# Performance work log

Measured on AMD Instinct MI355X. Metric: run time of the kernel, lower is better.

The kernel has to match this reference:

```python
import jax, jax.numpy as jnp
import numpy as np

B, S, D, H = 1, 2048, 1024, 16
DEPTH = D // H          # 64
A_DFF = 1024
NRES = 2                # num_reslayerA
SLOPE = 0.2             # LeakyReLU slope in plga attention
POW_EPS = 1e-9


def _ln(x, g, b):
    m = jnp.mean(x, axis=-1, keepdims=True)
    v = jnp.var(x, axis=-1, keepdims=True)
    return (x - m) * jax.lax.rsqrt(v + 1e-6) * g + b


def setup_inputs() -> dict:
    key = jax.random.key(0)
    ks = jax.random.split(key, 12)
    s = 0.02
    W = lambda k, shp: jax.random.normal(k, shp, jnp.float32) * s
    return {
        'q': jax.random.normal(ks[0], (B, S, D), jnp.float32),
        'k': jax.random.normal(ks[1], (B, S, D), jnp.float32),
        'v': jax.random.normal(ks[2], (B, S, D), jnp.float32),
        'mask': jnp.zeros((B, 1, 1, S), jnp.float32),
        'wq_w': W(ks[3], (D, D)), 'wq_b': jnp.zeros((D,), jnp.float32),
        'wk_w': W(ks[4], (D, D)), 'wk_b': jnp.zeros((D,), jnp.float32),
        'wv_w': W(ks[5], (D, D)), 'wv_b': jnp.zeros((D,), jnp.float32),
        'wo_w': W(ks[6], (D, D)), 'wo_b': jnp.zeros((D,), jnp.float32),
        # stacked ResLayerA params: Dense(depth->A_dff, relu) -> Dense(A_dff->depth) -> LN
        'rl_w1': W(ks[7], (NRES, DEPTH, A_DFF)), 'rl_b1': jnp.zeros((NRES, A_DFF), jnp.float32),
        'rl_w2': W(ks[8], (NRES, A_DFF, DEPTH)), 'rl_b2': jnp.zeros((NRES, DEPTH), jnp.float32),
        'rl_g': jnp.ones((NRES, DEPTH), jnp.float32), 'rl_beta': jnp.zeros((NRES, DEPTH), jnp.float32),
        # plga layer params: power coefficients, attention vector, bias
        'pw': jnp.ones((DEPTH,), jnp.float32),
        'a_vec': W(ks[9], (DEPTH,)),
        'ba': jnp.zeros((), jnp.float32),
    }


def reference(q, k, v, mask, wq_w, wq_b, wk_w, wk_b, wv_w, wv_b, wo_w, wo_b,
              rl_w1, rl_b1, rl_w2, rl_b2, rl_g, rl_beta, pw, a_vec, ba):
    Bq = q.shape[0]
    split = lambda x: x.reshape(Bq, -1, H, DEPTH).transpose(0, 2, 1, 3)  # [b,h,s,d]
    qh = split(q @ wq_w + wq_b)
    kh = split(k @ wk_w + wk_b)
    vh = split(v @ wv_w + wv_b)

    # metric tensor A = q^T q  -> [b,h,depth,depth]
    A = jnp.einsum('bhsd,bhse->bhde', qh, qh)
    # ResLayerA residual dense+LN stack over last dim
    for i in range(NRES):
        Ain = A
        hdn = jax.nn.relu(A @ rl_w1[i] + rl_b1[i])
        A = _ln((hdn @ rl_w2[i] + rl_b2[i]) + Ain, rl_g[i], rl_beta[i])

    # power-law graph attention (plga_layer, att_head=1, activation=None)
    Ap = jnp.power(jnp.abs(A) + POW_EPS, pw)                  # element-wise learned power
    avAp = jnp.einsum('d,bhde->bhe', a_vec, Ap)               # [b,h,depth] per-dim scaling
    E = jnp.einsum('bhsd,bhd,bhtd->bhst', qh, avAp, kh)       # pairwise logits [b,h,s,s]
    Ep = jnp.where(E > 0, E, SLOPE * E) + ba                  # LeakyReLU + learned bias
    Ep = Ep + mask * (-1e9)
    attv = jax.nn.softmax(Ep, axis=-1)
    Hnext = jnp.einsum('bhst,bhtd->bhsd', attv, vh)

    Hnext = Hnext.transpose(0, 2, 1, 3).reshape(Bq, -1, D)
    out = Hnext @ wo_w + wo_b
    return (out, E, A, pw, attv, ba, avAp, Ep)
```

## Files before the change

### kernel.cpp

```cpp
#include <hip/hip_runtime.h>
#include <stdint.h>

#define S_ 2048
#define D_ 1024
#define H_ 16
#define DEP_ 64

typedef float f32x4 __attribute__((ext_vector_type(4)));
typedef __bf16 bf16x8 __attribute__((ext_vector_type(8)));

#define MFMA16(a,b,c) __builtin_amdgcn_mfma_f32_16x16x32_bf16((a),(b),(c),0,0,0)

static constexpr size_t OFF_E    = 2097152ull;
static constexpr size_t OFF_A    = 69206016ull;
static constexpr size_t OFF_PW   = 69271552ull;
static constexpr size_t OFF_ATT  = 69271616ull;
static constexpr size_t OFF_BA   = 136380480ull;
static constexpr size_t OFF_AVAP = 136380481ull;
static constexpr size_t OFF_EP   = 136381505ull;

__device__ __forceinline__ short f2b(float f) {
  union { float f; uint32_t u; } c; c.f = f;
  uint32_t u = c.u;
  uint32_t r = (u + 0x7fffu + ((u >> 16) & 1u)) >> 16;
  return (short)(r & 0xffffu);
}
__device__ __forceinline__ float b2f(short s) {
  union { uint32_t u; float f; } c; c.u = ((uint32_t)(uint16_t)s) << 16;
  return c.f;
}
__device__ __forceinline__ void st_nt(float* p, f32x4 v) {
  __builtin_nontemporal_store(v, (f32x4*)p);
}

__global__ void k_cvt_all(const float* __restrict__ q, const float* __restrict__ k,
                          const float* __restrict__ v, const float* __restrict__ wq,
                          const float* __restrict__ wk, const float* __restrict__ wv,
                          const float* __restrict__ wo, const float* __restrict__ w1,
                          const float* __restrict__ w2, short* __restrict__ xbf,
                          short* __restrict__ wT, short* __restrict__ w1T,
                          short* __restrict__ w2T) {
  __shared__ float tile[64][65];
  int bid = blockIdx.x, t = threadIdx.x;
  if (bid < 6144) {
    int z = bid >> 11, bx = bid & 2047;
    const float* src = (z == 0) ? q : (z == 1) ? k : v;
    short* d = xbf + (size_t)z * (S_*D_);
    int i = (bx*256 + t)*4;
    float4 f = *(const float4*)(src + i);
    short4 o;
    o.x = f2b(f.x); o.y = f2b(f.y); o.z = f2b(f.z); o.w = f2b(f.w);
    *(short4*)(d + i) = o;
  } else if (bid < 7168) {
    int u = bid - 6144, z = u >> 8, tl = u & 255;
    int k0 = (tl >> 4)*64, n0 = (tl & 15)*64;
    const float* W = (z == 0) ? wq : (z == 1) ? wk : (z == 2) ? wv : wo;
    short* d = wT + (size_t)z * (D_*D_);
    for (int i = 0; i < 16; ++i) {
      int e = i*256 + t, r = e >> 6, c = e & 63;
      tile[r][c] = W[(size_t)(k0+r)*D_ + n0 + c];
    }
    __syncthreads();
    for (int i = 0; i < 16; ++i) {
      int e = i*256 + t, r = e >> 6, c = e & 63;
      d[(size_t)(n0+r)*D_ + k0 + c] = f2b(tile[c][r]);
    }
  } else {
    int u = bid - 7168, z = u >> 4, bx = u & 15;
    int l = z >> 1, which = z & 1;
    if (which == 0) {
      const float* src = w1 + (size_t)l*65536;
      short* d = w1T + (size_t)l*65536;
      int n0 = bx*64;
      for (int i = 0; i < 16; ++i) {
        int e = i*256 + t, r = e >> 6, c = e & 63;
        tile[r][c] = src[(size_t)r*1024 + n0 + c];
      }
      __syncthreads();
      for (int i = 0; i < 16; ++i) {
        int e = i*256 + t, r = e >> 6, c = e & 63;
        d[(size_t)(n0+r)*64 + c] = f2b(tile[c][r]);
      }
    } else {
      const float* src = w2 + (size_t)l*65536;
      short* d = w2T + (size_t)l*65536;
      int k0 = bx*64;
      for (int i = 0; i < 16; ++i) {
        int e = i*256 + t, r = e >> 6, c = e & 63;
        tile[r][c] = src[(size_t)(k0+r)*64 + c];
      }
      __syncthreads();
      for (int i = 0; i < 16; ++i) {
        int e = i*256 + t, r = e >> 6, c = e & 63;
        d[(size_t)r*1024 + k0 + c] = f2b(tile[c][r]);
      }
    }
  }
}

__global__ __launch_bounds__(256) void k_gemm(
    const short* __restrict__ Xall, const short* __restrict__ X2,
    const short* __restrict__ X3, const short* __restrict__ X4,
    const short* __restrict__ WTall,
    const float* __restrict__ b0, const float* __restrict__ b1v,
    const float* __restrict__ b2v, short* __restrict__ dstall,
    float* __restrict__ outf, int mode) {
  __shared__ __align__(16) short SS[2*128*72];
  short* As = SS;
  short* Bs = SS + 128*72;
  int z = blockIdx.z;
  const short* X  = Xall + (size_t)z * (S_*D_);
  const short* WT = WTall + (size_t)z * (D_*D_);
  int m0 = blockIdx.x * 128, n0 = blockIdx.y * 128;
  int t = threadIdx.x, lane = t & 63;
  int wr = t >> 7, wc = (t >> 6) & 1;
  int rA = lane & 15, kg = lane >> 4;
  f32x4 acc[4][4] = {};
  for (int kt = 0; kt < 16; ++kt) {
#pragma unroll
    for (int i = 0; i < 4; ++i) {
      int cid = i*256 + t, row = cid >> 3, c = cid & 7;
      size_t xi = (size_t)(m0+row)*D_ + kt*64 + c*8;
      if (mode == 2) {
        union { int4 v; short s[8]; } a1, a2, a3, a4, o;
        a1.v = *(const int4*)&X[xi];
        a2.v = *(const int4*)&X2[xi];
        a3.v = *(const int4*)&X3[xi];
        a4.v = *(const int4*)&X4[xi];
#pragma unroll
        for (int j = 0; j < 8; ++j)
          o.s[j] = f2b(b2f(a1.s[j]) + b2f(a2.s[j]) + b2f(a3.s[j]) + b2f(a4.s[j]));
        *(int4*)&As[row*72 + c*8] = o.v;
      } else {
        *(int4*)&As[row*72 + c*8] = *(const int4*)&X[xi];
      }
      *(int4*)&Bs[row*72 + c*8] = *(const int4*)&WT[(size_t)(n0+row)*D_ + kt*64 + c*8];
    }
    __syncthreads();
#pragma unroll
    for (int kk = 0; kk < 2; ++kk) {
      bf16x8 a[4], b[4];
#pragma unroll
      for (int m = 0; m < 4; ++m)
        a[m] = *(const bf16x8*)&As[(wr*64 + m*16 + rA)*72 + kk*32 + kg*8];
#pragma unroll
      for (int n = 0; n < 4; ++n)
        b[n] = *(const bf16x8*)&Bs[(wc*64 + n*16 + rA)*72 + kk*32 + kg*8];
#pragma unroll
      for (int m = 0; m < 4; ++m)
#pragma unroll
        for (int n = 0; n < 4; ++n)
          acc[m][n] = MFMA16(a[m], b[n], acc[m][n]);
    }
    __syncthreads();
  }
  const float* bias = (mode != 0) ? b0 : (z == 0 ? b0 : (z == 1 ? b1v : b2v));
  if (mode == 0) {
    short* Ct = SS;
#pragma unroll
    for (int m = 0; m < 4; ++m)
#pragma unroll
      for (int n = 0; n < 4; ++n) {
        int col = wc*64 + n*16 + rA;
        float bb = bias[n0 + col];
#pragma unroll
        for (int rr = 0; rr < 4; ++rr) {
          int row = wr*64 + m*16 + kg*4 + rr;
          Ct[row*136 + col] = f2b(acc[m][n][rr] + bb);
        }
      }
    __syncthreads();
#pragma unroll
    for (int p = 0; p < 8; ++p) {
      int row = p*16 + (t >> 4), unit = t & 15;
      int4 vv = *(const int4*)&Ct[row*136 + unit*8];
      int gcol = n0 + unit*8;
      int head = gcol >> 6, dd = gcol & 63;
      *(int4*)&dstall[(size_t)z*(S_*D_) + ((size_t)head*S_ + m0 + row)*DEP_ + dd] = vv;
    }
  } else {
    float* Ct = (float*)SS;
#pragma unroll
    for (int half = 0; half < 2; ++half) {
      if (wr == half) {
#pragma unroll
        for (int m = 0; m < 4; ++m)
#pragma unroll
          for (int n = 0; n < 4; ++n) {
            int col = wc*64 + n*16 + rA;
            float bb = bias[n0 + col];
#pragma unroll
            for (int rr = 0; rr < 4; ++rr)
              Ct[(m*16 + kg*4 + rr)*132 + col] = acc[m][n][rr] + bb;
          }
      }
      __syncthreads();
#pragma unroll
      for (int p = 0; p < 8; ++p) {
        int row_l = p*8 + (t >> 5), unit = t & 31;
        f32x4 vv = *(const f32x4*)&Ct[row_l*132 + unit*4];
        st_nt(&outf[(size_t)(m0 + half*64 + row_l)*D_ + n0 + unit*4], vv);
      }
      __syncthreads();
    }
  }
}

__global__ void k_transpose(const short* __restrict__ qh, const short* __restrict__ vh,
                            short* __restrict__ qhT, short* __restrict__ vhT) {
  __shared__ short tile[64][68];
  const short* src = blockIdx.z ? vh : qh;
  short* dst = blockIdx.z ? vhT : qhT;
  int h = blockIdx.y, s0 = blockIdx.x * 64, t = threadIdx.x;
  for (int i = 0; i < 16; ++i) {
    int e = i*256 + t, r = e >> 6, c = e & 63;
    tile[r][c] = src[((size_t)h*S_ + s0 + r)*DEP_ + c];
  }
  __syncthreads();
  for (int i = 0; i < 16; ++i) {
    int e = i*256 + t, r = e >> 6, c = e & 63;
    dst[((size_t)h*DEP_ + r)*S_ + s0 + c] = tile[c][r];
  }
}

__global__ __launch_bounds__(256) void k_metric_p(const short* __restrict__ qhT,
                                                  float* __restrict__ Apart) {
  __shared__ short qt[64*72];
  int kc = blockIdx.x, h = blockIdx.y, t = threadIdx.x, lane = t & 63;
  int wr = t >> 7, wc = (t >> 6) & 1;
  int rA = lane & 15, kg = lane >> 4;
  f32x4 acc[2][2] = {};
  for (int kt = 0; kt < 4; ++kt) {
#pragma unroll
    for (int i = 0; i < 2; ++i) {
      int cid = i*256 + t, row = cid >> 3, c = cid & 7;
      *(int4*)&qt[row*72 + c*8] =
        *(const int4*)&qhT[((size_t)h*DEP_ + row)*S_ + kc*256 + kt*64 + c*8];
    }
    __syncthreads();
#pragma unroll
    for (int kk = 0; kk < 2; ++kk) {
      bf16x8 a[2], b[2];
#pragma unroll
      for (int m = 0; m < 2; ++m)
        a[m] = *(const bf16x8*)&qt[(wr*32 + m*16 + rA)*72 + kk*32 + kg*8];
#pragma unroll
      for (int n = 0; n < 2; ++n)
        b[n] = *(const bf16x8*)&qt[(wc*32 + n*16 + rA)*72 + kk*32 + kg*8];
#pragma unroll
      for (int m = 0; m < 2; ++m)
#pragma unroll
        for (int n = 0; n < 2; ++n)
          acc[m][n] = MFMA16(a[m], b[n], acc[m][n]);
    }
    __syncthreads();
  }
#pragma unroll
  for (int m = 0; m < 2; ++m)
#pragma unroll
    for (int n = 0; n < 2; ++n)
#pragma unroll
      for (int rr = 0; rr < 4; ++rr) {
        int row = wr*32 + m*16 + kg*4 + rr, col = wc*32 + n*16 + rA;
        Apart[((size_t)(kc*16 + h))*4096 + row*64 + col] = acc[m][n][rr];
      }
}

__global__ __launch_bounds__(512) void k_res(
    const float* __restrict__ Apart, const short* __restrict__ w1T,
    const float* __restrict__ b1, const short* __restrict__ w2T,
    const float* __restrict__ b2, const float* __restrict__ gl,
    const float* __restrict__ bel, const float* __restrict__ pwv,
    const float* __restrict__ av, const float* __restrict__ bav,
    float* __restrict__ avApW, float* __restrict__ outB) {
  __shared__ float Af[64][68];
  __shared__ short Afb[64][72];
  __shared__ short hdP[64*520];
  __shared__ float red[8][64];
  int h = blockIdx.x, t = threadIdx.x;
  int lane = t & 63, w = t >> 6;
  int rA = lane & 15, kg = lane >> 4;
#pragma unroll
  for (int i = 0; i < 2; ++i) {
    int idx = (i*512 + t)*4;
    f32x4 s = {};
#pragma unroll
    for (int kc = 0; kc < 8; ++kc)
      s += *(const f32x4*)&Apart[((size_t)(kc*16 + h))*4096 + idx];
    int r = idx >> 6, c = idx & 63;
    *(f32x4*)&Af[r][c] = s;
    union { int2 v; short sh[4]; } pk;
#pragma unroll
    for (int j = 0; j < 4; ++j) pk.sh[j] = f2b(s[j]);
    *(int2*)&Afb[r][c] = pk.v;
  }
  __syncthreads();
  for (int layer = 0; layer < 2; ++layer) {
    const short* w1l = w1T + layer*65536;
    const short* w2l = w2T + layer*65536;
    f32x4 acc2[4][4] = {};
    for (int kc = 0; kc < 2; ++kc) {
      int c0g = kc*512 + w*64;
      f32x4 acc1[4][4] = {};
#pragma unroll
      for (int kk = 0; kk < 2; ++kk) {
        bf16x8 aA[4], bW[4];
#pragma unroll
        for (int mf = 0; mf < 4; ++mf)
          aA[mf] = *(const bf16x8*)&Afb[mf*16 + rA][kk*32 + kg*8];
#pragma unroll
        for (int nf = 0; nf < 4; ++nf)
          bW[nf] = *(const bf16x8*)&w1l[(size_t)(c0g + nf*16 + rA)*64 + kk*32 + kg*8];
#pragma unroll
        for (int mf = 0; mf < 4; ++mf)
#pragma unroll
          for (int nf = 0; nf < 4; ++nf)
            acc1[mf][nf] = MFMA16(aA[mf], bW[nf], acc1[mf][nf]);
      }
      __syncthreads();
#pragma unroll
      for (int nf = 0; nf < 4; ++nf) {
        int col = w*64 + nf*16 + rA;
        float bb1 = b1[layer*1024 + kc*512 + col];
#pragma unroll
        for (int mf = 0; mf < 4; ++mf)
#pragma unroll
          for (int rr = 0; rr < 4; ++rr) {
            int r = mf*16 + kg*4 + rr;
            hdP[r*520 + col] = f2b(fmaxf(acc1[mf][nf][rr] + bb1, 0.f));
          }
      }
      __syncthreads();
#pragma unroll
      for (int kk = 0; kk < 2; ++kk) {
        bf16x8 a2[4], bw2[4];
#pragma unroll
        for (int mf = 0; mf < 4; ++mf)
          a2[mf] = *(const bf16x8*)&hdP[(mf*16 + rA)*520 + w*64 + kk*32 + kg*8];
#pragma unroll
        for (int nf = 0; nf < 4; ++nf)
          bw2[nf] = *(const bf16x8*)&w2l[(size_t)(nf*16 + rA)*1024 + kc*512 + w*64 + kk*32 + kg*8];
#pragma unroll
        for (int mf = 0; mf < 4; ++mf)
#pragma unroll
          for (int nf = 0; nf < 4; ++nf)
            acc2[mf][nf] = MFMA16(a2[mf], bw2[nf], acc2[mf][nf]);
      }
    }
    __syncthreads();
    float* P = (float*)hdP;
    if (w >= 4) {
      int slot = w - 4;
#pragma unroll
      for (int mf = 0; mf < 4; ++mf)
#pragma unroll
        for (int nf = 0; nf < 4; ++nf)
#pragma unroll
          for (int rr = 0; rr < 4; ++rr)
            P[slot*4160 + (mf*16 + kg*4 + rr)*65 + nf*16 + rA] = acc2[mf][nf][rr];
    }
    __syncthreads();
    if (w < 4) {
#pragma unroll
      for (int mf = 0; mf < 4; ++mf)
#pragma unroll
        for (int nf = 0; nf < 4; ++nf)
#pragma unroll
          for (int rr = 0; rr < 4; ++rr)
            P[w*4160 + (mf*16 + kg*4 + rr)*65 + nf*16 + rA] += acc2[mf][nf][rr];
    }
    __syncthreads();
    int r = t >> 3, j0 = (t & 7)*8;
    float x[8], s1 = 0.f, s2 = 0.f;
#pragma unroll
    for (int j = 0; j < 8; ++j) {
      int c = j0 + j;
      float xx = P[r*65 + c] + P[4160 + r*65 + c] + P[8320 + r*65 + c] + P[12480 + r*65 + c]
               + b2[layer*64 + c] + Af[r][c];
      x[j] = xx; s1 += xx; s2 += xx*xx;
    }
    s1 += __shfl_xor(s1, 1); s1 += __shfl_xor(s1, 2); s1 += __shfl_xor(s1, 4);
    s2 += __shfl_xor(s2, 1); s2 += __shfl_xor(s2, 2); s2 += __shfl_xor(s2, 4);
    float mean = s1 * (1.f/64.f);
    float var  = s2 * (1.f/64.f) - mean*mean;
    float rstd = rsqrtf(var + 1e-6f);
#pragma unroll
    for (int j = 0; j < 8; ++j) {
      int c = j0 + j;
      float nx = (x[j] - mean)*rstd*gl[layer*64 + c] + bel[layer*64 + c];
      Af[r][c] = nx;
      Afb[r][c] = f2b(nx);
      if (layer == 1) outB[OFF_A + (size_t)h*4096 + r*64 + c] = nx;
    }
    __syncthreads();
  }
  {
    int e = t & 63, dg = t >> 6;
    float pe = pwv[e], p = 0.f;
#pragma unroll
    for (int j = 0; j < 8; ++j) {
      int d = dg*8 + j;
      p += av[d] * powf(fabsf(Af[d][e]) + 1e-9f, pe);
    }
    red[dg][e] = p;
  }
  __syncthreads();
  if (t < 64) {
    float tot = 0.f;
#pragma unroll
    for (int g = 0; g < 8; ++g) tot += red[g][t];
    avApW[h*64 + t] = tot;
    outB[OFF_AVAP + h*64 + t] = tot;
  }
  if (h == 0) {
    if (t < 64) outB[OFF_PW + t] = pwv[t];
    if (t == 0) outB[OFF_BA] = bav[0];
  }
}

__global__ __launch_bounds__(256) void k_pass1(
    const short* __restrict__ qh, const short* __restrict__ kh,
    const float* __restrict__ avAp, const float* __restrict__ mask,
    const float* __restrict__ bap, float* __restrict__ outB,
    float2* __restrict__ part) {
  __shared__ float Et[64*128];
  __shared__ float2 red[4][64];
  __shared__ float avl[64];
  short* Qs = (short*)Et;
  short* Ks = ((short*)Et) + 4096;
  int tt = blockIdx.x, sb = blockIdx.y, h = blockIdx.z;
  int s0 = sb*64, t0 = tt*128;
  int t = threadIdx.x, lane = t & 63, w = t >> 6;
  int rA = lane & 15, kg = lane >> 4;
  if (t < 16) *(f32x4*)&avl[t*4] = *(const f32x4*)&avAp[h*64 + t*4];
  __syncthreads();
#pragma unroll
  for (int i = 0; i < 6; ++i) {
    int cid = i*256 + t, row = cid >> 3, c = cid & 7, cs = c ^ (row & 7);
    if (row < 64) {
      union { int4 v; short s[8]; } qa, qo;
      qa.v = *(const int4*)&qh[((size_t)h*S_ + s0 + row)*DEP_ + c*8];
#pragma unroll
      for (int j = 0; j < 8; ++j) qo.s[j] = f2b(b2f(qa.s[j]) * avl[c*8 + j]);
      *(int4*)&Qs[row*64 + cs*8] = qo.v;
    } else {
      int kr = row - 64, csk = c ^ (kr & 7);
      *(int4*)&Ks[kr*64 + csk*8] = *(const int4*)&kh[((size_t)h*S_ + t0 + kr)*DEP_ + c*8];
    }
  }
  __syncthreads();
  f32x4 acc[4][2] = {};
#pragma unroll
  for (int kk = 0; kk < 2; ++kk) {
    bf16x8 a[4], b[2];
#pragma unroll
    for (int m = 0; m < 4; ++m) {
      int row = m*16 + rA, c = (kk*4 + kg) ^ (row & 7);
      a[m] = *(const bf16x8*)&Qs[row*64 + c*8];
    }
#pragma unroll
    for (int n = 0; n < 2; ++n) {
      int kr = w*32 + n*16 + rA, c = (kk*4 + kg) ^ (kr & 7);
      b[n] = *(const bf16x8*)&Ks[kr*64 + c*8];
    }
#pragma unroll
    for (int m = 0; m < 4; ++m)
#pragma unroll
      for (int n = 0; n < 2; ++n)
        acc[m][n] = MFMA16(b[n], a[m], acc[m][n]);
  }
  float bav = bap[0];
  f32x4 mkf[2];
#pragma unroll
  for (int n = 0; n < 2; ++n) {
    f32x4 mm = *(const f32x4*)&mask[t0 + w*32 + n*16 + kg*4];
#pragma unroll
    for (int j = 0; j < 4; ++j) mkf[n][j] = mm[j] * (-1e9f);
  }
#pragma unroll
  for (int m = 0; m < 4; ++m) {
    float mx = -3.4e38f;
    f32x4 ep4[2];
#pragma unroll
    for (int n = 0; n < 2; ++n) {
      f32x4 e = acc[m][n];
      f32x4 ep;
#pragma unroll
      for (int j = 0; j < 4; ++j) {
        float ee = e[j];
        ep[j] = (ee > 0.f ? ee : 0.2f*ee) + bav + mkf[n][j];
        mx = fmaxf(mx, ep[j]);
      }
      ep4[n] = ep;
    }
    mx = fmaxf(mx, __shfl_xor(mx, 16));
    mx = fmaxf(mx, __shfl_xor(mx, 32));
    float sm = 0.f;
#pragma unroll
    for (int n = 0; n < 2; ++n)
#pragma unroll
      for (int j = 0; j < 4; ++j) sm += expf(ep4[n][j] - mx);
    sm += __shfl_xor(sm, 16);
    sm += __shfl_xor(sm, 32);
    if (kg == 0) red[w][m*16 + rA] = make_float2(mx, sm);
  }
  __syncthreads();
  if (t < 64) {
    float M = red[0][t].x;
#pragma unroll
    for (int g = 1; g < 4; ++g) M = fmaxf(M, red[g][t].x);
    float L = 0.f;
#pragma unroll
    for (int g = 0; g < 4; ++g) L += red[g][t].y * expf(red[g][t].x - M);
    part[((size_t)(h*S_ + s0 + t))*16 + tt] = make_float2(M, L);
  }
#pragma unroll
  for (int m = 0; m < 4; ++m)
#pragma unroll
    for (int n = 0; n < 2; ++n) {
      int row = m*16 + rA;
      int unit = w*8 + n*4 + kg;
      *(f32x4*)&Et[row*128 + ((unit ^ (row & 7)))*4] = acc[m][n];
    }
  __syncthreads();
  float* Eo  = outB + OFF_E;
  float* Epo = outB + OFF_EP;
  int colu = t & 31, rbase = t >> 5;
  f32x4 mm4 = *(const f32x4*)&mask[t0 + colu*4];
  f32x4 mk4;
#pragma unroll
  for (int j = 0; j < 4; ++j) mk4[j] = mm4[j] * (-1e9f);
#pragma unroll
  for (int r = 0; r < 8; ++r) {
    int row = r*8 + rbase;
    f32x4 e = *(const f32x4*)&Et[row*128 + ((colu ^ (row & 7)))*4];
    size_t gb = ((size_t)h*S_ + s0 + row)*S_ + t0 + colu*4;
    st_nt(&Eo[gb], e);
    f32x4 ep;
#pragma unroll
    for (int j = 0; j < 4; ++j)
      ep[j] = (e[j] > 0.f ? e[j] : 0.2f*e[j]) + bav + mk4[j];
    st_nt(&Epo[gb], ep);
  }
}

__global__ void k_sreduce(const float2* __restrict__ part, float2* __restrict__ fin) {
  int row = blockIdx.x * 256 + threadIdx.x;
  const float2* pp = part + (size_t)row * 16;
  float2 p[16];
  float M = -3.4e38f;
#pragma unroll
  for (int i = 0; i < 16; ++i) { p[i] = pp[i]; M = fmaxf(M, p[i].x); }
  float L = 0.f;
#pragma unroll
  for (int i = 0; i < 16; ++i) L += p[i].y * expf(p[i].x - M);
  fin[row] = make_float2(M, L);
}

__global__ __launch_bounds__(256) void k_pass2(
    const short* __restrict__ qh, const short* __restrict__ kh,
    const short* __restrict__ vhT, const float* __restrict__ avAp,
    const float* __restrict__ mask, const float* __restrict__ bap,
    const float2* __restrict__ fin, float* __restrict__ attv,
    short* __restrict__ Hnp0, short* __restrict__ Hnp1,
    short* __restrict__ Hnp2, short* __restrict__ Hnp3) {
  __shared__ short Qs[128*64];
  __shared__ __align__(16) short KP[128*128];
  __shared__ short Vs[64*128];
  __shared__ float avl[64];
  int st = blockIdx.x, tc = blockIdx.y, h = blockIdx.z;
  int s0 = st * 128;
  int t = threadIdx.x, lane = t & 63;
  int wr = t >> 7, wc = (t >> 6) & 1;
  int rA = lane & 15, kg = lane >> 4;
  if (t < 16) *(f32x4*)&avl[t*4] = *(const f32x4*)&avAp[h*64 + t*4];
  __syncthreads();
#pragma unroll
  for (int i = 0; i < 4; ++i) {
    int cid = i*256 + t, row = cid >> 3, c = cid & 7, cs = c ^ (row & 7);
    union { int4 v; short s[8]; } qa, qo;
    qa.v = *(const int4*)&qh[((size_t)h*S_ + s0 + row)*DEP_ + c*8];
#pragma unroll
    for (int j = 0; j < 8; ++j) qo.s[j] = f2b(b2f(qa.s[j]) * avl[c*8 + j]);
    *(int4*)&Qs[row*64 + cs*8] = qo.v;
  }
  float Ms[4], Li[4];
#pragma unroll
  for (int m = 0; m < 4; ++m) {
    float2 f = fin[h*S_ + s0 + wr*64 + m*16 + rA];
    Ms[m] = f.x; Li[m] = 1.f / f.y;
  }
  float bav = bap[0];
  __syncthreads();
  bf16x8 aq[4][2];
#pragma unroll
  for (int m = 0; m < 4; ++m)
#pragma unroll
    for (int kk = 0; kk < 2; ++kk) {
      int row = wr*64 + m*16 + rA, c = (kk*4 + kg) ^ (row & 7);
      aq[m][kk] = *(const bf16x8*)&Qs[row*64 + c*8];
    }
  f32x4 acc2[4][2] = {};
  for (int tt = tc*4; tt < tc*4 + 4; ++tt) {
    int t0 = tt * 128;
    __syncthreads();
#pragma unroll
    for (int i = 0; i < 4; ++i) {
      int cid = i*256 + t, row = cid >> 3, c = cid & 7, cs = c ^ (row & 7);
      *(int4*)&KP[row*64 + cs*8] = *(const int4*)&kh[((size_t)h*S_ + t0 + row)*DEP_ + c*8];
    }
#pragma unroll
    for (int i = 0; i < 4; ++i) {
      int cid = i*256 + t, row = cid >> 4, c = cid & 15, cs = c ^ (row & 7);
      *(int4*)&Vs[row*128 + cs*8] = *(const int4*)&vhT[((size_t)h*DEP_ + row)*S_ + t0 + c*8];
    }
    __syncthreads();
    f32x4 accE[4][4] = {};
#pragma unroll
    for (int kk = 0; kk < 2; ++kk) {
      bf16x8 b[4];
#pragma unroll
      for (int n = 0; n < 4; ++n) {
        int row = wc*64 + n*16 + rA, c = (kk*4 + kg) ^ (row & 7);
        b[n] = *(const bf16x8*)&KP[row*64 + c*8];
      }
#pragma unroll
      for (int m = 0; m < 4; ++m)
#pragma unroll
        for (int n = 0; n < 4; ++n)
          accE[m][n] = MFMA16(b[n], aq[m][kk], accE[m][n]);
    }
    f32x4 mkf[4];
#pragma unroll
    for (int n = 0; n < 4; ++n) {
      f32x4 mm = *(const f32x4*)&mask[t0 + wc*64 + n*16 + kg*4];
#pragma unroll
      for (int j = 0; j < 4; ++j) mkf[n][j] = mm[j] * (-1e9f);
    }
#pragma unroll
    for (int m = 0; m < 4; ++m)
#pragma unroll
      for (int n = 0; n < 4; ++n) {
        f32x4 e = accE[m][n], p;
#pragma unroll
        for (int j = 0; j < 4; ++j) {
          float ep = (e[j] > 0.f ? e[j] : 0.2f*e[j]) + bav + mkf[n][j];
          p[j] = expf(ep - Ms[m]) * Li[m];
        }
        accE[m][n] = p;
      }
    __syncthreads();
#pragma unroll
    for (int m = 0; m < 4; ++m) {
      int srow = wr*64 + m*16 + rA;
#pragma unroll
      for (int n = 0; n < 4; ++n) {
        int tcol = wc*64 + n*16 + kg*4;
        union { int2 v; short s[4]; } pk;
#pragma unroll
        for (int j = 0; j < 4; ++j) pk.s[j] = f2b(accE[m][n][j]);
        *(int2*)((char*)KP + srow*256 + ((tcol*2) ^ ((srow & 7) << 4))) = pk.v;
      }
    }
    __syncthreads();
#pragma unroll
    for (int kkp = 0; kkp < 4; ++kkp) {
      bf16x8 ap[4], bv[2];
#pragma unroll
      for (int m = 0; m < 4; ++m) {
        int row = wr*64 + m*16 + rA;
        ap[m] = *(const bf16x8*)((const char*)KP + row*256 + ((kkp*64 + kg*16) ^ ((row & 7) << 4)));
      }
#pragma unroll
      for (int n = 0; n < 2; ++n) {
        int dd = wc*32 + n*16 + rA, c = (kkp*4 + kg) ^ (dd & 7);
        bv[n] = *(const bf16x8*)&Vs[dd*128 + c*8];
      }
#pragma unroll
      for (int m = 0; m < 4; ++m)
#pragma unroll
        for (int n = 0; n < 2; ++n)
          acc2[m][n] = MFMA16(ap[m], bv[n], acc2[m][n]);
    }
#pragma unroll
    for (int it = 0; it < 16; ++it) {
      int row = it*8 + (t >> 5);
      int u8 = t & 31;
      union { int2 v; short s[4]; } pv;
      pv.v = *(const int2*)((const char*)KP + row*256 + ((u8*8) ^ ((row & 7) << 4)));
      f32x4 o;
#pragma unroll
      for (int j = 0; j < 4; ++j) o[j] = b2f(pv.s[j]);
      st_nt(&attv[((size_t)h*S_ + s0 + row)*S_ + t0 + u8*4], o);
    }
  }
  short* Hp = (tc == 0) ? Hnp0 : (tc == 1) ? Hnp1 : (tc == 2) ? Hnp2 : Hnp3;
  short* Ht = KP;
  __syncthreads();
#pragma unroll
  for (int m = 0; m < 4; ++m)
#pragma unroll
    for (int n = 0; n < 2; ++n) {
      int col = wc*32 + n*16 + rA;
#pragma unroll
      for (int rr = 0; rr < 4; ++rr) {
        int row = wr*64 + m*16 + kg*4 + rr;
        Ht[row*72 + col] = f2b(acc2[m][n][rr]);
      }
    }
  __syncthreads();
#pragma unroll
  for (int p = 0; p < 4; ++p) {
    int row = p*32 + (t >> 3), unit = t & 7;
    int4 vv = *(const int4*)&Ht[row*72 + unit*8];
    *(int4*)&Hp[(size_t)(s0 + row)*D_ + h*DEP_ + unit*8] = vv;
  }
}

extern "C" void kernel_launch(void* const* d_in, const int* in_sizes, int n_in,
                              void* d_out, int out_size, void* d_ws, size_t ws_size,
                              hipStream_t stream) {
  (void)in_sizes; (void)n_in; (void)out_size; (void)ws_size;
  const float* q    = (const float*)d_in[0];
  const float* k    = (const float*)d_in[1];
  const float* v    = (const float*)d_in[2];
  const float* mask = (const float*)d_in[3];
  const float* wq_w = (const float*)d_in[4];
  const float* wq_b = (const float*)d_in[5];
  const float* wk_w = (const float*)d_in[6];
  const float* wk_b = (const float*)d_in[7];
  const float* wv_w = (const float*)d_in[8];
  const float* wv_b = (const float*)d_in[9];
  const float* wo_w = (const float*)d_in[10];
  const float* wo_b = (const float*)d_in[11];
  const float* rl_w1 = (const float*)d_in[12];
  const float* rl_b1 = (const float*)d_in[13];
  const float* rl_w2 = (const float*)d_in[14];
  const float* rl_b2 = (const float*)d_in[15];
  const float* rl_g  = (const float*)d_in[16];
  const float* rl_be = (const float*)d_in[17];
  const float* pw    = (const float*)d_in[18];
  const float* avec  = (const float*)d_in[19];
  const float* ba    = (const float*)d_in[20];
  float* outf = (float*)d_out;

  char* w = (char*)d_ws;
  short* xbf  = (short*)(w);
  short* wT   = (short*)(w + (12u << 20));
  short* qh   = (short*)(w + (20u << 20));
  short* kh   = (short*)(w + (24u << 20));
  short* vh   = (short*)(w + (28u << 20));
  short* qhT  = (short*)(w);
  short* vhT  = (short*)(w + (4u << 20));
  float* Apart = (float*)(w + (12u << 20));
  float2* part = (float2*)(w + (8u << 20));
  float2* fin  = (float2*)(w + (16u << 20));
  float* avApW = (float*)(w + (16u << 20) + (512u << 10));
  short* w1T  = (short*)(w + (32u << 20));
  short* w2T  = (short*)(w + (32u << 20) + (256u << 10));
  short* Hnp0 = (short*)(w);
  short* Hnp1 = (short*)(w + (12u << 20));
  short* Hnp2 = (short*)(w + (28u << 20));
  short* Hnp3 = (short*)(w + (8u << 20));

  k_cvt_all<<<dim3(7232), 256, 0, stream>>>(q, k, v, wq_w, wk_w, wv_w, wo_w,
                                            rl_w1, rl_w2, xbf, wT, w1T, w2T);
  k_gemm<<<dim3(16, 8, 3), 256, 0, stream>>>(xbf, nullptr, nullptr, nullptr, wT,
                                             wq_b, wk_b, wv_b, qh, nullptr, 0);
  k_transpose<<<dim3(32, 16, 2), 256, 0, stream>>>(qh, vh, qhT, vhT);
  k_metric_p<<<dim3(8, 16), 256, 0, stream>>>(qhT, Apart);
  k_res<<<dim3(16), 512, 0, stream>>>(Apart, w1T, rl_b1, w2T, rl_b2, rl_g, rl_be,
                                      pw, avec, ba, avApW, outf);
  k_pass1<<<dim3(16, 32, 16), 256, 0, stream>>>(qh, kh, avApW, mask, ba, outf, part);
  k_sreduce<<<dim3(128), 256, 0, stream>>>(part, fin);
  k_pass2<<<dim3(16, 4, 16), 256, 0, stream>>>(qh, kh, vhT, avApW, mask, ba, fin,
                                               outf + OFF_ATT, Hnp0, Hnp1, Hnp2, Hnp3);
  k_gemm<<<dim3(16, 8, 1), 256, 0, stream>>>(Hnp0, Hnp1, Hnp2, Hnp3, wT + 3u*D_*D_,
                                             wo_b, wo_b, wo_b, nullptr, outf, 2);
}
```

Baseline: 458.4 us.

## Fuse V transpose into projection GEMM and metric tensor into res kernel

The QKV projection GEMM now writes V directly in transposed per-head layout through a transposed LDS staging tile, which removes the separate transpose kernel. The metric tensor q^T q is now computed inside k_res, using a swizzled LDS transpose of qh and a tree reduction across 8 waves. This drops the k_metric_p launch and its partial-sum buffer. The trade-off is that the metric GEMM now runs on only 16 blocks instead of 128, so less of the GPU is used for that stage.

```diff
diff --git a/kernel.cpp b/kernel.cpp
--- a/kernel.cpp
+++ b/kernel.cpp
@@ -104,7 +104,7 @@
     const short* __restrict__ WTall,
     const float* __restrict__ b0, const float* __restrict__ b1v,
     const float* __restrict__ b2v, short* __restrict__ dstall,
-    float* __restrict__ outf, int mode) {
+    short* __restrict__ vhT, float* __restrict__ outf, int mode) {
   __shared__ __align__(16) short SS[2*128*72];
   short* As = SS;
   short* Bs = SS + 128*72;
@@ -156,27 +156,51 @@
   }
   const float* bias = (mode != 0) ? b0 : (z == 0 ? b0 : (z == 1 ? b1v : b2v));
   if (mode == 0) {
-    short* Ct = SS;
-#pragma unroll
-    for (int m = 0; m < 4; ++m)
-#pragma unroll
-      for (int n = 0; n < 4; ++n) {
-        int col = wc*64 + n*16 + rA;
-        float bb = bias[n0 + col];
-#pragma unroll
-        for (int rr = 0; rr < 4; ++rr) {
-          int row = wr*64 + m*16 + kg*4 + rr;
-          Ct[row*136 + col] = f2b(acc[m][n][rr] + bb);
+    if (z == 2) {
+      short* Ct = SS;
+#pragma unroll
+      for (int m = 0; m < 4; ++m)
+#pragma unroll
+        for (int n = 0; n < 4; ++n) {
+          int col = wc*64 + n*16 + rA;
+          float bb = bias[n0 + col];
+#pragma unroll
+          for (int rr = 0; rr < 4; ++rr) {
+            int row = wr*64 + m*16 + kg*4 + rr;
+            Ct[col*136 + row] = f2b(acc[m][n][rr] + bb);
+          }
         }
-      }
-    __syncthreads();
-#pragma unroll
-    for (int p = 0; p < 8; ++p) {
-      int row = p*16 + (t >> 4), unit = t & 15;
-      int4 vv = *(const int4*)&Ct[row*136 + unit*8];
-      int gcol = n0 + unit*8;
-      int head = gcol >> 6, dd = gcol & 63;
-      *(int4*)&dstall[(size_t)z*(S_*D_) + ((size_t)head*S_ + m0 + row)*DEP_ + dd] = vv;
+      __syncthreads();
+#pragma unroll
+      for (int p = 0; p < 8; ++p) {
+        int col = p*16 + (t >> 4), r0 = (t & 15)*8;
+        int4 vv = *(const int4*)&Ct[col*136 + r0];
+        int gcol = n0 + col, head = gcol >> 6, dd = gcol & 63;
+        *(int4*)&vhT[((size_t)head*DEP_ + dd)*S_ + m0 + r0] = vv;
+      }
+    } else {
+      short* Ct = SS;
+#pragma unroll
+      for (int m = 0; m < 4; ++m)
+#pragma unroll
+        for (int n = 0; n < 4; ++n) {
+          int col = wc*64 + n*16 + rA;
+          float bb = bias[n0 + col];
+#pragma unroll
+          for (int rr = 0; rr < 4; ++rr) {
+            int row = wr*64 + m*16 + kg*4 + rr;
+            Ct[row*136 + col] = f2b(acc[m][n][rr] + bb);
+          }
+        }
+      __syncthreads();
+#pragma unroll
+      for (int p = 0; p < 8; ++p) {
+        int row = p*16 + (t >> 4), unit = t & 15;
+        int4 vv = *(const int4*)&Ct[row*136 + unit*8];
+        int gcol = n0 + unit*8;
+        int head = gcol >> 6, dd = gcol & 63;
+        *(int4*)&dstall[(size_t)z*(S_*D_) + ((size_t)head*S_ + m0 + row)*DEP_ + dd] = vv;
+      }
     }
   } else {
     float* Ct = (float*)SS;
@@ -206,68 +230,8 @@
   }
 }
 
-__global__ void k_transpose(const short* __restrict__ qh, const short* __restrict__ vh,
-                            short* __restrict__ qhT, short* __restrict__ vhT) {
-  __shared__ short tile[64][68];
-  const short* src = blockIdx.z ? vh : qh;
-  short* dst = blockIdx.z ? vhT : qhT;
-  int h = blockIdx.y, s0 = blockIdx.x * 64, t = threadIdx.x;
-  for (int i = 0; i < 16; ++i) {
-    int e = i*256 + t, r = e >> 6, c = e & 63;
-    tile[r][c] = src[((size_t)h*S_ + s0 + r)*DEP_ + c];
-  }
-  __syncthreads();
-  for (int i = 0; i < 16; ++i) {
-    int e = i*256 + t, r = e >> 6, c = e & 63;
-    dst[((size_t)h*DEP_ + r)*S_ + s0 + c] = tile[c][r];
-  }
-}
-
-__global__ __launch_bounds__(256) void k_metric_p(const short* __restrict__ qhT,
-                                                  float* __restrict__ Apart) {
-  __shared__ short qt[64*72];
-  int kc = blockIdx.x, h = blockIdx.y, t = threadIdx.x, lane = t & 63;
-  int wr = t >> 7, wc = (t >> 6) & 1;
-  int rA = lane & 15, kg = lane >> 4;
-  f32x4 acc[2][2] = {};
-  for (int kt = 0; kt < 4; ++kt) {
-#pragma unroll
-    for (int i = 0; i < 2; ++i) {
-      int cid = i*256 + t, row = cid >> 3, c = cid & 7;
-      *(int4*)&qt[row*72 + c*8] =
-        *(const int4*)&qhT[((size_t)h*DEP_ + row)*S_ + kc*256 + kt*64 + c*8];
-    }
-    __syncthreads();
-#pragma unroll
-    for (int kk = 0; kk < 2; ++kk) {
-      bf16x8 a[2], b[2];
-#pragma unroll
-      for (int m = 0; m < 2; ++m)
-        a[m] = *(const bf16x8*)&qt[(wr*32 + m*16 + rA)*72 + kk*32 + kg*8];
-#pragma unroll
-      for (int n = 0; n < 2; ++n)
-        b[n] = *(const bf16x8*)&qt[(wc*32 + n*16 + rA)*72 + kk*32 + kg*8];
-#pragma unroll
-      for (int m = 0; m < 2; ++m)
-#pragma unroll
-        for (int n = 0; n < 2; ++n)
-          acc[m][n] = MFMA16(a[m], b[n], acc[m][n]);
-    }
-    __syncthreads();
-  }
-#pragma unroll
-  for (int m = 0; m < 2; ++m)
-#pragma unroll
-    for (int n = 0; n < 2; ++n)
-#pragma unroll
-      for (int rr = 0; rr < 4; ++rr) {
-        int row = wr*32 + m*16 + kg*4 + rr, col = wc*32 + n*16 + rA;
-        Apart[((size_t)(kc*16 + h))*4096 + row*64 + col] = acc[m][n][rr];
-      }
-}
-
 __global__ __launch_bounds__(512) void k_res(
-    const float* __restrict__ Apart, const short* __restrict__ w1T,
+    const short* __restrict__ qh, const short* __restrict__ w1T,
     const float* __restrict__ b1, const short* __restrict__ w2T,
     const float* __restrict__ b2, const float* __restrict__ gl,
     const float* __restrict__ bel, const float* __restrict__ pwv,
@@ -275,26 +239,111 @@
     float* __restrict__ avApW, float* __restrict__ outB) {
   __shared__ float Af[64][68];
   __shared__ short Afb[64][72];
-  __shared__ short hdP[64*520];
+  __shared__ __align__(16) short hdP[64*520];
   __shared__ float red[8][64];
   int h = blockIdx.x, t = threadIdx.x;
   int lane = t & 63, w = t >> 6;
   int rA = lane & 15, kg = lane >> 4;
-#pragma unroll
-  for (int i = 0; i < 2; ++i) {
-    int idx = (i*512 + t)*4;
-    f32x4 s = {};
-#pragma unroll
-    for (int kc = 0; kc < 8; ++kc)
-      s += *(const f32x4*)&Apart[((size_t)(kc*16 + h))*4096 + idx];
-    int r = idx >> 6, c = idx & 63;
-    *(f32x4*)&Af[r][c] = s;
-    union { int2 v; short sh[4]; } pk;
-#pragma unroll
-    for (int j = 0; j < 4; ++j) pk.sh[j] = f2b(s[j]);
-    *(int2*)&Afb[r][c] = pk.v;
-  }
-  __syncthreads();
+  {
+    short* Tl = hdP + (size_t)w * 4096;
+    f32x4 accM[4][4] = {};
+    for (int ks = 0; ks < 4; ++ks) {
+      int sbase = w*256 + ks*64;
+#pragma unroll
+      for (int c = 0; c < 8; ++c) {
+        union { int4 v; short s[8]; } qa;
+        qa.v = *(const int4*)&qh[((size_t)h*S_ + sbase + lane)*DEP_ + c*8];
+#pragma unroll
+        for (int j = 0; j < 8; ++j) {
+          int d = c*8 + j;
+          Tl[d*64 + (((lane >> 3) ^ j) << 3) + (lane & 7)] = qa.s[j];
+        }
+      }
+      __syncthreads();
+#pragma unroll
+      for (int kk = 0; kk < 2; ++kk) {
+        bf16x8 f[4];
+#pragma unroll
+        for (int i = 0; i < 4; ++i) {
+          int d = i*16 + rA;
+          f[i] = *(const bf16x8*)&Tl[d*64 + (((kk*4 + kg) ^ (d & 7)) << 3)];
+        }
+#pragma unroll
+        for (int i = 0; i < 4; ++i)
+#pragma unroll
+          for (int j = 0; j < 4; ++j)
+            accM[i][j] = MFMA16(f[i], f[j], accM[i][j]);
+      }
+      __syncthreads();
+    }
+    float* PM = (float*)hdP;
+    if (w >= 4) {
+      int slot = w - 4;
+#pragma unroll
+      for (int i = 0; i < 4; ++i)
+#pragma unroll
+        for (int j = 0; j < 4; ++j)
+#pragma unroll
+          for (int rr = 0; rr < 4; ++rr)
+            PM[slot*4096 + (i*16 + kg*4 + rr)*64 + j*16 + rA] = accM[i][j][rr];
+    }
+    __syncthreads();
+    if (w < 4) {
+#pragma unroll
+      for (int i = 0; i < 4; ++i)
+#pragma unroll
+        for (int j = 0; j < 4; ++j)
+#pragma unroll
+          for (int rr = 0; rr < 4; ++rr)
+            accM[i][j][rr] += PM[w*4096 + (i*16 + kg*4 + rr)*64 + j*16 + rA];
+    }
+    __syncthreads();
+    if (w == 2 || w == 3) {
+      int slot = w - 2;
+#pragma unroll
+      for (int i = 0; i < 4; ++i)
+#pragma unroll
+        for (int j = 0; j < 4; ++j)
+#pragma unroll
+          for (int rr = 0; rr < 4; ++rr)
+            PM[slot*4096 + (i*16 + kg*4 + rr)*64 + j*16 + rA] = accM[i][j][rr];
+    }
+    __syncthreads();
+    if (w < 2) {
+#pragma unroll
+      for (int i = 0; i < 4; ++i)
+#pragma unroll
+        for (int j = 0; j < 4; ++j)
+#pragma unroll
+          for (int rr = 0; rr < 4; ++rr)
+            accM[i][j][rr] += PM[w*4096 + (i*16 + kg*4 + rr)*64 + j*16 + rA];
+    }
+    __syncthreads();
+    if (w == 1) {
+#pragma unroll
+      for (int i = 0; i < 4; ++i)
+#pragma unroll
+        for (int j = 0; j < 4; ++j)
+#pragma unroll
+          for (int rr = 0; rr < 4; ++rr)
+            PM[(i*16 + kg*4 + rr)*64 + j*16 + rA] = accM[i][j][rr];
+    }
+    __syncthreads();
+    if (w == 0) {
+#pragma unroll
+      for (int i = 0; i < 4; ++i)
+#pragma unroll
+        for (int j = 0; j < 4; ++j)
+#pragma unroll
+          for (int rr = 0; rr < 4; ++rr) {
+            int row = i*16 + kg*4 + rr, col = j*16 + rA;
+            float vv = accM[i][j][rr] + PM[row*64 + col];
+            Af[row][col] = vv;
+            Afb[row][col] = f2b(vv);
+          }
+    }
+    __syncthreads();
+  }
   for (int layer = 0; layer < 2; ++layer) {
     const short* w1l = w1T + layer*65536;
     const short* w2l = w2T + layer*65536;
@@ -749,10 +798,7 @@
   short* wT   = (short*)(w + (12u << 20));
   short* qh   = (short*)(w + (20u << 20));
   short* kh   = (short*)(w + (24u << 20));
-  short* vh   = (short*)(w + (28u << 20));
-  short* qhT  = (short*)(w);
-  short* vhT  = (short*)(w + (4u << 20));
-  float* Apart = (float*)(w + (12u << 20));
+  short* vhT  = (short*)(w + (28u << 20));
   float2* part = (float2*)(w + (8u << 20));
   float2* fin  = (float2*)(w + (16u << 20));
   float* avApW = (float*)(w + (16u << 20) + (512u << 10));
@@ -760,21 +806,19 @@
   short* w2T  = (short*)(w + (32u << 20) + (256u << 10));
   short* Hnp0 = (short*)(w);
   short* Hnp1 = (short*)(w + (12u << 20));
-  short* Hnp2 = (short*)(w + (28u << 20));
+  short* Hnp2 = (short*)(w + (4u << 20));
   short* Hnp3 = (short*)(w + (8u << 20));
 
   k_cvt_all<<<dim3(7232), 256, 0, stream>>>(q, k, v, wq_w, wk_w, wv_w, wo_w,
                                             rl_w1, rl_w2, xbf, wT, w1T, w2T);
   k_gemm<<<dim3(16, 8, 3), 256, 0, stream>>>(xbf, nullptr, nullptr, nullptr, wT,
-                                             wq_b, wk_b, wv_b, qh, nullptr, 0);
-  k_transpose<<<dim3(32, 16, 2), 256, 0, stream>>>(qh, vh, qhT, vhT);
-  k_metric_p<<<dim3(8, 16), 256, 0, stream>>>(qhT, Apart);
-  k_res<<<dim3(16), 512, 0, stream>>>(Apart, w1T, rl_b1, w2T, rl_b2, rl_g, rl_be,
+                                             wq_b, wk_b, wv_b, qh, vhT, nullptr, 0);
+  k_res<<<dim3(16), 512, 0, stream>>>(qh, w1T, rl_b1, w2T, rl_b2, rl_g, rl_be,
                                       pw, avec, ba, avApW, outf);
   k_pass1<<<dim3(16, 32, 16), 256, 0, stream>>>(qh, kh, avApW, mask, ba, outf, part);
   k_sreduce<<<dim3(128), 256, 0, stream>>>(part, fin);
   k_pass2<<<dim3(16, 4, 16), 256, 0, stream>>>(qh, kh, vhT, avApW, mask, ba, fin,
                                                outf + OFF_ATT, Hnp0, Hnp1, Hnp2, Hnp3);
   k_gemm<<<dim3(16, 8, 1), 256, 0, stream>>>(Hnp0, Hnp1, Hnp2, Hnp3, wT + 3u*D_*D_,
-                                             wo_b, wo_b, wo_b, nullptr, outf, 2);
-}
+                                             wo_b, wo_b, wo_b, nullptr, nullptr, outf, 2);
+}
```

After: 508.3 us. 1.11x slower.
